# Optimization experiments

Measured on AMD Instinct MI355X. Metric: run time of the kernel, lower is better.

The kernel has to match this reference:

```python
import jax, jax.numpy as jnp
import numpy as np

BETA = 0.95
THRESH = 1.0
T = 25
MAXD = 11      # dilated_kernel_size: 250//25=10 -> bumped to odd 11
LP = 10        # left_pad = 250//25
B = 1024
SIGINIT = 5.0  # max_delay // 2, SIG is frozen at this value


@jax.custom_vjp
def atan_spike(u):
    # heaviside forward, atan surrogate gradient (snntorch surrogate.atan, alpha=2)
    return (u > 0).astype(u.dtype)

def _atan_fwd(u):
    return atan_spike(u), u

def _atan_bwd(u, g):
    return (g / (1.0 + (jnp.pi * u) ** 2),)

atan_spike.defvjp(_atan_fwd, _atan_bwd)


def dcls_kernel(W, P, SIG):
    # DCLS 'gauss': gaussian-interpolated dense kernel.
    # W: (O, I, kc), P/SIG: (1, O, I, kc) -> dense kernel (O, I, MAXD)
    idx = jnp.arange(MAXD, dtype=W.dtype)
    Pc = P[0] + MAXD // 2                      # center positions in dense kernel
    S = jnp.abs(SIG[0]) + 0.27                 # sigma floor (DCLS epsilon)
    X = jnp.exp(-0.5 * ((idx[:, None, None, None] - Pc) / S) ** 2)  # (K,O,I,kc)
    X = X / (X.sum(axis=0, keepdims=True) + 1e-7)
    return jnp.einsum('oic,joic->oij', W, X)


def dcls_conv(x, W, P, SIG, b):
    # x: (B, C_in, L) -> (B, C_out, L - MAXD + 1), VALID conv like padding=0
    k = dcls_kernel(W, P, SIG)
    y = jax.lax.conv_general_dilated(x, k, (1,), 'VALID',
                                     dimension_numbers=('NCH', 'OIH', 'NCH'))
    return y + b[None, :, None]


def batchnorm(x, gamma, beta, mean, var, eps=1e-5):
    # eval-mode BatchNorm1d over (B, C, L)
    inv = gamma / jnp.sqrt(var + eps)
    return (x - mean[None, :, None]) * inv[None, :, None] + beta[None, :, None]


def lif_scan(x):
    # snntorch Leaky, reset_mechanism='subtract'; x: (B, C, T) input currents
    xT = jnp.moveaxis(x, 2, 0)  # (T, B, C)

    def step(mem, xt):
        reset = jax.lax.stop_gradient(atan_spike(mem - THRESH))  # detached reset
        mem = BETA * mem + xt - reset * THRESH
        spk = atan_spike(mem - THRESH)
        return mem, (spk, mem)

    _, (spk, mem) = jax.lax.scan(step, jnp.zeros_like(xT[0]), xT)
    return spk, mem  # each (T, B, C)


def pad_left(x):
    return jnp.pad(x, ((0, 0), (0, 0), (LP, 0)))


def setup_inputs() -> dict:
    key = jax.random.key(0)
    ks = jax.random.split(key, 16)

    def w_init(k, o, i):
        return jax.random.normal(k, (o, i, 1), jnp.float32) / np.sqrt(i)

    inp = {
        'data': jax.random.normal(ks[0], (B, T, 140), jnp.float32),
        'W1': w_init(ks[1], 256, 140),
        'b1': jax.random.normal(ks[2], (256,), jnp.float32) * 0.01,
        'P1': jax.random.uniform(ks[3], (1, 256, 140, 1), jnp.float32, -SIGINIT, SIGINIT),
        'SIG1': jnp.full((1, 256, 140, 1), SIGINIT, jnp.float32),
        'bn1_gamma': jax.random.uniform(ks[4], (256,), jnp.float32, 0.5, 1.5),
        'bn1_beta': jax.random.normal(ks[5], (256,), jnp.float32) * 0.1,
        'bn1_mean': jax.random.normal(ks[6], (256,), jnp.float32) * 0.1,
        'bn1_var': jax.random.uniform(ks[7], (256,), jnp.float32, 0.5, 1.5),
        'W2': w_init(ks[8], 256, 256),
        'b2': jax.random.normal(ks[9], (256,), jnp.float32) * 0.01,
        'P2': jax.random.uniform(ks[10], (1, 256, 256, 1), jnp.float32, -SIGINIT, SIGINIT),
        'SIG2': jnp.full((1, 256, 256, 1), SIGINIT, jnp.float32),
        'bn2_gamma': jax.random.uniform(ks[11], (256,), jnp.float32, 0.5, 1.5),
        'bn2_beta': jax.random.normal(ks[12], (256,), jnp.float32) * 0.1,
        'bn2_mean': jax.random.normal(ks[13], (256,), jnp.float32) * 0.1,
        'bn2_var': jax.random.uniform(ks[14], (256,), jnp.float32, 0.5, 1.5),
        'W3': w_init(ks[15], 20, 256),
        'b3': jnp.zeros((20,), jnp.float32),
        'P3': jax.random.uniform(jax.random.fold_in(key, 99), (1, 20, 256, 1), jnp.float32, -SIGINIT, SIGINIT),
        'SIG3': jnp.full((1, 20, 256, 1), SIGINIT, jnp.float32),
    }
    return inp


def reference(data, W1, b1, P1, SIG1, bn1_gamma, bn1_beta, bn1_mean, bn1_var,
              W2, b2, P2, SIG2, bn2_gamma, bn2_beta, bn2_mean, bn2_var,
              W3, b3, P3, SIG3):
    # data: (B, T, 140); pad time dim on the left, then to (B, C, L)
    x = jnp.moveaxis(jnp.pad(data, ((0, 0), (LP, 0), (0, 0))), 1, 2)  # (B,140,T+LP)
    x = batchnorm(dcls_conv(x, W1, P1, SIG1, b1), bn1_gamma, bn1_beta, bn1_mean, bn1_var)
    spk1, _ = lif_scan(x)                  # (T, B, 256)
    in1 = jnp.moveaxis(spk1, 0, 2)         # (B, 256, T)  (dropout eval = identity)

    x = batchnorm(dcls_conv(pad_left(in1), W2, P2, SIG2, b2),
                  bn2_gamma, bn2_beta, bn2_mean, bn2_var)
    spk2, _ = lif_scan(x)
    in2 = jnp.moveaxis(spk2, 0, 2)         # (B, 256, T)

    x = dcls_conv(pad_left(in2), W3, P3, SIG3, b3)  # (B, 20, T)
    spk3, mem3 = lif_scan(x)               # (T, B, 20) each
    return spk3, mem3
```

## Files before the change

kernel.cpp:

```cpp
#include <hip/hip_runtime.h>
#include <math.h>

#define BB 1024
#define TT 25
#define LP 10
#define MAXD 11

#define XR2 26
#define XC 264
#define XSZ2 (XR2 * XC)

#define IC1 140
#define ICP1 160
#define XC1 168
#define XSZ1 (XR2 * XC1)
#define SS1 (2 * XSZ1)

typedef __bf16 bf16x8 __attribute__((ext_vector_type(8)));
typedef float  f32x4  __attribute__((ext_vector_type(4)));

#define MFMA16(A, B, C) __builtin_amdgcn_mfma_f32_16x16x32_bf16((A), (B), (C), 0, 0, 0)

__global__ void gen_trip(const float* __restrict__ W,
                         const float* __restrict__ P,
                         const float* __restrict__ SIG,
                         __bf16* __restrict__ Khi, __bf16* __restrict__ Kmid,
                         __bf16* __restrict__ Klo,
                         int O, int Opad, int I, int Ipad) {
    int idx = blockIdx.x * blockDim.x + threadIdx.x;
    if (idx >= Opad * Ipad) return;
    int i = idx % Ipad;
    int o = idx / Ipad;
    if (o >= O || i >= I) {
#pragma unroll
        for (int j = 0; j < MAXD; ++j) {
            size_t ofs = ((size_t)(j * Opad + o)) * Ipad + i;
            Khi[ofs] = (__bf16)0.0f;
            Kmid[ofs] = (__bf16)0.0f;
            Klo[ofs] = (__bf16)0.0f;
        }
        return;
    }
    int widx = o * I + i;
    float w  = W[widx];
    float pc = P[widx] + (float)(MAXD / 2);
    float s  = fabsf(SIG[widx]) + 0.27f;
    float x[MAXD];
    float sum = 0.f;
#pragma unroll
    for (int j = 0; j < MAXD; ++j) {
        float d = ((float)j - pc) / s;
        x[j] = expf(-0.5f * d * d);
        sum += x[j];
    }
    float denom = sum + 1e-7f;
#pragma unroll
    for (int j = 0; j < MAXD; ++j) {
        float kv = w * (x[j] / denom);
        __bf16 h = (__bf16)kv;
        float  r1 = kv - (float)h;
        __bf16 m = (__bf16)r1;
        float  r2 = r1 - (float)m;
        __bf16 l = (__bf16)r2;
        size_t ofs = ((size_t)(j * Opad + o)) * Ipad + i;
        Khi[ofs] = h;
        Kmid[ofs] = m;
        Klo[ofs] = l;
    }
}

__global__ __launch_bounds__(512, 2)
void conv1_mfma(const float* __restrict__ xin,
                const __bf16* __restrict__ Khi,
                const __bf16* __restrict__ Kmid,
                const __bf16* __restrict__ Klo,
                const float* __restrict__ bias,
                const float* __restrict__ gamma,
                const float* __restrict__ beta,
                const float* __restrict__ mean,
                const float* __restrict__ var,
                __bf16* __restrict__ spk1) {
    __shared__ __align__(16) char smem[3 * SS1 * 2];
    __bf16* xs = (__bf16*)smem;
    float*  ys = (float*)smem;

    const int rr = blockIdx.x & 7;
    const int gg = blockIdx.x >> 3;
    const int pp = 2 * (rr + 8 * (gg >> 1)) + (gg & 1);
    const int b0 = pp * 2;

    const int tid  = threadIdx.x;
    const int w    = tid >> 6;
    const int lane = tid & 63;
    const int lm   = lane & 15;
    const int quad = lane >> 4;

    {
        uint32_t* xz = (uint32_t*)smem;
        for (int k = tid; k < 3 * SS1 / 2; k += 512) xz[k] = 0u;
    }
    __syncthreads();
#pragma unroll
    for (int bl = 0; bl < 2; ++bl) {
        const float* src = xin + (size_t)(b0 + bl) * (TT * IC1);
        for (int k = tid; k < TT * IC1; k += 512) {
            int t = k / IC1;
            int i = k - t * IC1;
            float x  = src[k];
            __bf16 h = (__bf16)x;
            float r1 = x - (float)h;
            __bf16 m = (__bf16)r1;
            float r2 = r1 - (float)m;
            __bf16 l = (__bf16)r2;
            int ofs = bl * XSZ1 + t * XC1 + i;
            xs[0 * SS1 + ofs] = h;
            xs[1 * SS1 + ofs] = m;
            xs[2 * SS1 + ofs] = l;
        }
    }
    __syncthreads();

    f32x4 acc[2][4];
#pragma unroll
    for (int p = 0; p < 2; ++p)
#pragma unroll
        for (int nt = 0; nt < 4; ++nt) acc[p][nt] = (f32x4){0.f, 0.f, 0.f, 0.f};

    auto loadA = [&](int n, bf16x8* Ah, bf16x8* Am, bf16x8* Al) {
        n = (n > 54) ? 54 : n;
        const int j = n / 5;
        const int ic = n - 5 * j;
        const size_t base =
            (size_t)(j * 256 + w * 32 + lm) * ICP1 + ic * 32 + quad * 8;
#pragma unroll
        for (int p = 0; p < 2; ++p) {
            Ah[p] = *(const bf16x8*)(Khi  + base + p * 16 * ICP1);
            Am[p] = *(const bf16x8*)(Kmid + base + p * 16 * ICP1);
            Al[p] = *(const bf16x8*)(Klo  + base + p * 16 * ICP1);
        }
    };

    auto step = [&](int n, bf16x8* Ah, bf16x8* Am, bf16x8* Al) {
        const int j = n / 5;
        const int ic = n - 5 * j;
        int r0 = lm + j - 10;          r0 = ((unsigned)r0 < 25u) ? r0 : 25;
        int r1 = 16 + lm + j - 10;     r1 = ((unsigned)r1 < 25u) ? r1 : 25;
        const int col = ic * 32 + quad * 8;
#pragma unroll
        for (int bl = 0; bl < 2; ++bl) {
            bf16x8 Bh[2], Bm[2], Bl[2];
#pragma unroll
            for (int th = 0; th < 2; ++th) {
                const int row = th ? r1 : r0;
                const int ofs = bl * XSZ1 + row * XC1 + col;
                Bh[th] = *(const bf16x8*)&xs[0 * SS1 + ofs];
                Bm[th] = *(const bf16x8*)&xs[1 * SS1 + ofs];
                Bl[th] = *(const bf16x8*)&xs[2 * SS1 + ofs];
            }
#pragma unroll
            for (int p = 0; p < 2; ++p)
#pragma unroll
                for (int th = 0; th < 2; ++th)
                    acc[p][bl * 2 + th] = MFMA16(Ah[p], Bh[th], acc[p][bl * 2 + th]);
#pragma unroll
            for (int p = 0; p < 2; ++p)
#pragma unroll
                for (int th = 0; th < 2; ++th)
                    acc[p][bl * 2 + th] = MFMA16(Ah[p], Bm[th], acc[p][bl * 2 + th]);
#pragma unroll
            for (int p = 0; p < 2; ++p)
#pragma unroll
                for (int th = 0; th < 2; ++th)
                    acc[p][bl * 2 + th] = MFMA16(Am[p], Bh[th], acc[p][bl * 2 + th]);
#pragma unroll
            for (int p = 0; p < 2; ++p)
#pragma unroll
                for (int th = 0; th < 2; ++th)
                    acc[p][bl * 2 + th] = MFMA16(Ah[p], Bl[th], acc[p][bl * 2 + th]);
#pragma unroll
            for (int p = 0; p < 2; ++p)
#pragma unroll
                for (int th = 0; th < 2; ++th)
                    acc[p][bl * 2 + th] = MFMA16(Am[p], Bm[th], acc[p][bl * 2 + th]);
#pragma unroll
            for (int p = 0; p < 2; ++p)
#pragma unroll
                for (int th = 0; th < 2; ++th)
                    acc[p][bl * 2 + th] = MFMA16(Al[p], Bh[th], acc[p][bl * 2 + th]);
        }
    };

    bf16x8 A0h[2], A0m[2], A0l[2], A1h[2], A1m[2], A1l[2];
    loadA(0, A0h, A0m, A0l);
    for (int n = 0; n < 54; n += 2) {
        loadA(n + 1, A1h, A1m, A1l);
        step(n, A0h, A0m, A0l);
        loadA(n + 2, A0h, A0m, A0l);
        step(n + 1, A1h, A1m, A1l);
    }
    step(54, A0h, A0m, A0l);

#pragma unroll
    for (int bl = 0; bl < 2; ++bl) {
        __syncthreads();
#pragma unroll
        for (int p = 0; p < 2; ++p)
#pragma unroll
            for (int th = 0; th < 2; ++th) {
                int t = th * 16 + lm;
                if (t < TT) {
                    int ob = w * 32 + p * 16 + quad * 4;
#pragma unroll
                    for (int v = 0; v < 4; ++v)
                        ys[(ob + v) * 27 + t] = acc[p][bl * 2 + th][v];
                }
            }
        __syncthreads();
        if (tid < 256) {
            const int o = tid;
            float scale = gamma[o] / sqrtf(var[o] + 1e-5f);
            float ofs   = (bias[o] - mean[o]) * scale + beta[o];
            unsigned short* dst =
                (unsigned short*)spk1 + (size_t)(b0 + bl) * (TT * 256) + o;
            const float* yrow = &ys[o * 27];
            float memv = 0.f;
#pragma unroll
            for (int t = 0; t < TT; ++t) {
                float a     = yrow[t] * scale + ofs;
                float reset = (memv > 1.0f) ? 1.0f : 0.f;
                memv        = 0.95f * memv + a - reset;
                dst[t * 256] = (memv > 1.0f) ? 0x3F80 : 0;
            }
        }
    }
}

__global__ __launch_bounds__(512, 2)
void conv23_mfma(const __bf16* __restrict__ spk1,
                 const __bf16* __restrict__ Khi,
                 const __bf16* __restrict__ Kmid,
                 const __bf16* __restrict__ Klo,
                 const float* __restrict__ bias,
                 const float* __restrict__ gamma,
                 const float* __restrict__ beta,
                 const float* __restrict__ mean,
                 const float* __restrict__ var,
                 const __bf16* __restrict__ K3hi,
                 const __bf16* __restrict__ K3mid,
                 const __bf16* __restrict__ K3lo,
                 const float* __restrict__ b3,
                 float* __restrict__ out) {
    __shared__ __align__(16) char smem[61568];
    __bf16* xs  = (__bf16*)smem;
    float*  ysq = (float*)(smem + 54912);
    float*  ys3 = (float*)smem;

    const int b0   = blockIdx.x * 4;
    const int tid  = threadIdx.x;
    const int w    = tid >> 6;
    const int lane = tid & 63;
    const int lm   = lane & 15;
    const int quad = lane >> 4;

    for (int k = tid; k < 4 * (XC / 2); k += 512) {
        int bl = k / (XC / 2);
        int c  = k % (XC / 2);
        ((uint32_t*)xs)[(bl * XSZ2 + 25 * XC) / 2 + c] = 0u;
    }
    for (int k = tid; k < 4 * 800; k += 512) {
        int bl = k / 800;
        int v  = k % 800;
        int t  = v >> 5;
        int iv = v & 31;
        uint4 d = ((const uint4*)(spk1 + (size_t)(b0 + bl) * (TT * 256)))[v];
        *(uint4*)&xs[bl * XSZ2 + t * XC + iv * 8] = d;
    }
    __syncthreads();

    f32x4 acc[2][8];
#pragma unroll
    for (int pi = 0; pi < 2; ++pi)
#pragma unroll
        for (int nt = 0; nt < 8; ++nt) acc[pi][nt] = (f32x4){0.f, 0.f, 0.f, 0.f};

    {
        auto loadA = [&](int n, bf16x8* Ah, bf16x8* Am, bf16x8* Al) {
            n = (n > 87) ? 87 : n;
            const int j = n >> 3, ic = n & 7;
#pragma unroll
            for (int pi = 0; pi < 2; ++pi) {
                const size_t base =
                    (size_t)(j * 256 + w * 32 + pi * 16 + lm) * 256 + ic * 32 + quad * 8;
                Ah[pi] = *(const bf16x8*)(Khi  + base);
                Am[pi] = *(const bf16x8*)(Kmid + base);
                Al[pi] = *(const bf16x8*)(Klo  + base);
            }
        };
        auto loadB = [&](int n, bf16x8* Bf) {
            const int j = n >> 3, ic = n & 7;
            int r0 = lm + j - 10;          r0 = ((unsigned)r0 < 25u) ? r0 : 25;
            int r1 = 16 + lm + j - 10;     r1 = ((unsigned)r1 < 25u) ? r1 : 25;
            const int col = ic * 32 + quad * 8;
#pragma unroll
            for (int bl = 0; bl < 4; ++bl) {
                Bf[bl * 2 + 0] = *(const bf16x8*)&xs[bl * XSZ2 + r0 * XC + col];
                Bf[bl * 2 + 1] = *(const bf16x8*)&xs[bl * XSZ2 + r1 * XC + col];
            }
        };
        auto compute = [&](bf16x8* Ah, bf16x8* Am, bf16x8* Al, bf16x8* Bf) {
#pragma unroll
            for (int pi = 0; pi < 2; ++pi)
#pragma unroll
                for (int nt = 0; nt < 8; ++nt)
                    acc[pi][nt] = MFMA16(Ah[pi], Bf[nt], acc[pi][nt]);
#pragma unroll
            for (int pi = 0; pi < 2; ++pi)
#pragma unroll
                for (int nt = 0; nt < 8; ++nt)
                    acc[pi][nt] = MFMA16(Am[pi], Bf[nt], acc[pi][nt]);
#pragma unroll
            for (int pi = 0; pi < 2; ++pi)
#pragma unroll
                for (int nt = 0; nt < 8; ++nt)
                    acc[pi][nt] = MFMA16(Al[pi], Bf[nt], acc[pi][nt]);
        };

        bf16x8 A0h[2], A0m[2], A0l[2], A1h[2], A1m[2], A1l[2], B0[8], B1[8];
        loadA(0, A0h, A0m, A0l);
        loadB(0, B0);
        for (int n = 0; n < 86; n += 2) {
            loadA(n + 1, A1h, A1m, A1l);
            loadB(n + 1, B1);
            compute(A0h, A0m, A0l, B0);
            loadA(n + 2, A0h, A0m, A0l);
            loadB(n + 2, B0);
            compute(A1h, A1m, A1l, B1);
        }
        loadA(87, A1h, A1m, A1l);
        loadB(87, B1);
        compute(A0h, A0m, A0l, B0);
        compute(A1h, A1m, A1l, B1);
    }

#pragma unroll
    for (int bl = 0; bl < 4; ++bl) {
#pragma unroll
        for (int q = 0; q < 4; ++q) {
            __syncthreads();
            if ((w >> 1) == q) {
#pragma unroll
                for (int pi = 0; pi < 2; ++pi)
#pragma unroll
                    for (int th = 0; th < 2; ++th) {
                        int t = th * 16 + lm;
                        if (t < TT) {
                            int ol = (w & 1) * 32 + pi * 16 + quad * 4;
#pragma unroll
                            for (int v = 0; v < 4; ++v)
                                ysq[(ol + v) * 26 + t] = acc[pi][bl * 2 + th][v];
                        }
                    }
            }
            __syncthreads();
            if (tid < 64) {
                const int o = q * 64 + tid;
                float scale = gamma[o] / sqrtf(var[o] + 1e-5f);
                float ofs   = (bias[o] - mean[o]) * scale + beta[o];
                const float* yrow = &ysq[tid * 26];
                unsigned short* sx = (unsigned short*)xs;
                float memv = 0.f;
#pragma unroll
                for (int t = 0; t < TT; ++t) {
                    float a     = yrow[t] * scale + ofs;
                    float reset = (memv > 1.0f) ? 1.0f : 0.f;
                    memv        = 0.95f * memv + a - reset;
                    sx[bl * XSZ2 + t * XC + o] = (memv > 1.0f) ? 0x3F80 : 0;
                }
            }
        }
    }
    __syncthreads();

    {
        const int p3  = w >> 2;
        const int bl3 = w & 3;
        f32x4 accH[2], accM[2], accL[2];
#pragma unroll
        for (int th = 0; th < 2; ++th) {
            accH[th] = (f32x4){0.f, 0.f, 0.f, 0.f};
            accM[th] = (f32x4){0.f, 0.f, 0.f, 0.f};
            accL[th] = (f32x4){0.f, 0.f, 0.f, 0.f};
        }

        auto loadA3 = [&](int n, bf16x8* Ah, bf16x8* Am, bf16x8* Al) {
            n = (n > 87) ? 87 : n;
            const int j = n >> 3, ic = n & 7;
            const size_t kofs =
                ((size_t)(j * 32 + p3 * 16 + lm)) * 256 + ic * 32 + quad * 8;
            *Ah = *(const bf16x8*)(K3hi  + kofs);
            *Am = *(const bf16x8*)(K3mid + kofs);
            *Al = *(const bf16x8*)(K3lo  + kofs);
        };
        auto step3 = [&](int n, bf16x8 Ah, bf16x8 Am, bf16x8 Al) {
            const int j = n >> 3, ic = n & 7;
#pragma unroll
            for (int th = 0; th < 2; ++th) {
                int r = th * 16 + lm + j - 10;
                r = ((unsigned)r < 25u) ? r : 25;
                bf16x8 Bf =
                    *(const bf16x8*)&xs[bl3 * XSZ2 + r * XC + ic * 32 + quad * 8];
                accH[th] = MFMA16(Ah, Bf, accH[th]);
                accM[th] = MFMA16(Am, Bf, accM[th]);
                accL[th] = MFMA16(Al, Bf, accL[th]);
            }
        };

        bf16x8 A0h, A0m, A0l, A1h, A1m, A1l;
        loadA3(0, &A0h, &A0m, &A0l);
        for (int n = 0; n < 86; n += 2) {
            loadA3(n + 1, &A1h, &A1m, &A1l);
            step3(n, A0h, A0m, A0l);
            loadA3(n + 2, &A0h, &A0m, &A0l);
            step3(n + 1, A1h, A1m, A1l);
        }
        loadA3(87, &A1h, &A1m, &A1l);
        step3(86, A0h, A0m, A0l);
        step3(87, A1h, A1m, A1l);

        __syncthreads();
#pragma unroll
        for (int th = 0; th < 2; ++th) {
            int t = th * 16 + lm;
            if (t < TT) {
#pragma unroll
                for (int v = 0; v < 4; ++v)
                    ys3[(bl3 * 32 + p3 * 16 + quad * 4 + v) * 26 + t] =
                        accH[th][v] + accM[th][v] + accL[th][v];
            }
        }
        __syncthreads();

        if (tid < 80) {
            const int bl2 = tid / 20;
            const int o   = tid % 20;
            float memv = 0.f;
            float bo   = b3[o];
            const float* yrow = &ys3[(bl2 * 32 + o) * 26];
#pragma unroll
            for (int t = 0; t < TT; ++t) {
                float a     = yrow[t] + bo;
                float reset = (memv > 1.0f) ? 1.0f : 0.f;
                memv        = 0.95f * memv + a - reset;
                float spk   = (memv > 1.0f) ? 1.0f : 0.f;
                out[(t * BB + (b0 + bl2)) * 20 + o]               = spk;
                out[TT * BB * 20 + (t * BB + (b0 + bl2)) * 20 + o] = memv;
            }
        }
    }
}

extern "C" void kernel_launch(void* const* d_in, const int* in_sizes, int n_in,
                              void* d_out, int out_size, void* d_ws, size_t ws_size,
                              hipStream_t stream) {
    const float* data = (const float*)d_in[0];
    const float* W1   = (const float*)d_in[1];
    const float* b1   = (const float*)d_in[2];
    const float* P1   = (const float*)d_in[3];
    const float* SIG1 = (const float*)d_in[4];
    const float* g1   = (const float*)d_in[5];
    const float* be1  = (const float*)d_in[6];
    const float* m1   = (const float*)d_in[7];
    const float* v1   = (const float*)d_in[8];
    const float* W2   = (const float*)d_in[9];
    const float* b2   = (const float*)d_in[10];
    const float* P2   = (const float*)d_in[11];
    const float* SIG2 = (const float*)d_in[12];
    const float* g2   = (const float*)d_in[13];
    const float* be2  = (const float*)d_in[14];
    const float* m2   = (const float*)d_in[15];
    const float* v2   = (const float*)d_in[16];
    const float* W3   = (const float*)d_in[17];
    const float* b3   = (const float*)d_in[18];
    const float* P3   = (const float*)d_in[19];
    const float* SIG3 = (const float*)d_in[20];
    float* out = (float*)d_out;

    char* p = (char*)d_ws;
    __bf16* K1hi  = (__bf16*)p;  p += 901120;
    __bf16* K1mid = (__bf16*)p;  p += 901120;
    __bf16* K1lo  = (__bf16*)p;  p += 901120;
    __bf16* spk1  = (__bf16*)p;  p += 13107200;
    __bf16* K2hi  = (__bf16*)p;  p += 1441792;
    __bf16* K2mid = (__bf16*)p;  p += 1441792;
    __bf16* K2lo  = (__bf16*)p;  p += 1441792;
    __bf16* K3hi  = (__bf16*)p;  p += 180224;
    __bf16* K3mid = (__bf16*)p;  p += 180224;
    __bf16* K3lo  = (__bf16*)p;

    gen_trip<<<(256 * 160 + 255) / 256, 256, 0, stream>>>(
        W1, P1, SIG1, K1hi, K1mid, K1lo, 256, 256, 140, 160);
    gen_trip<<<(256 * 256 + 255) / 256, 256, 0, stream>>>(
        W2, P2, SIG2, K2hi, K2mid, K2lo, 256, 256, 256, 256);
    gen_trip<<<(32 * 256 + 255) / 256, 256, 0, stream>>>(
        W3, P3, SIG3, K3hi, K3mid, K3lo, 20, 32, 256, 256);

    conv1_mfma<<<BB / 2, 512, 0, stream>>>(data, K1hi, K1mid, K1lo,
                                           b1, g1, be1, m1, v1, spk1);
    conv23_mfma<<<BB / 4, 512, 0, stream>>>(spk1, K2hi, K2mid, K2lo,
                                            b2, g2, be2, m2, v2,
                                            K3hi, K3mid, K3lo, b3, out);
}
```

Baseline: 433.9 us.

## Double conv23 block to 1024 threads, splitting output channels across 16 waves

The fused conv2/conv3 kernel moves from 512 to 1024 threads per block. Each wave now owns 16 output channels instead of 32, which halves its accumulator registers and per-wave A-fragment loads. The conv3 stage is likewise split across time halves per wave. The aim is more waves per block for latency hiding and more MFMA parallelism. In exchange, each wave re-reads the same B fragments from shared memory (more LDS traffic per MFMA), the software double-buffering of B loads is dropped, and launch bounds now allow only one block per CU.

```diff
diff --git a/kernel.cpp b/kernel.cpp
--- a/kernel.cpp
+++ b/kernel.cpp
@@ -235,7 +235,7 @@
     }
 }
 
-__global__ __launch_bounds__(512, 2)
+__global__ __launch_bounds__(1024, 1)
 void conv23_mfma(const __bf16* __restrict__ spk1,
                  const __bf16* __restrict__ Khi,
                  const __bf16* __restrict__ Kmid,
@@ -262,12 +262,12 @@
     const int lm   = lane & 15;
     const int quad = lane >> 4;
 
-    for (int k = tid; k < 4 * (XC / 2); k += 512) {
+    for (int k = tid; k < 4 * (XC / 2); k += 1024) {
         int bl = k / (XC / 2);
         int c  = k % (XC / 2);
         ((uint32_t*)xs)[(bl * XSZ2 + 25 * XC) / 2 + c] = 0u;
     }
-    for (int k = tid; k < 4 * 800; k += 512) {
+    for (int k = tid; k < 4 * 800; k += 1024) {
         int bl = k / 800;
         int v  = k % 800;
         int t  = v >> 5;
@@ -277,69 +277,50 @@
     }
     __syncthreads();
 
-    f32x4 acc[2][8];
-#pragma unroll
-    for (int pi = 0; pi < 2; ++pi)
-#pragma unroll
-        for (int nt = 0; nt < 8; ++nt) acc[pi][nt] = (f32x4){0.f, 0.f, 0.f, 0.f};
+    f32x4 acc[8];
+#pragma unroll
+    for (int nt = 0; nt < 8; ++nt) acc[nt] = (f32x4){0.f, 0.f, 0.f, 0.f};
 
     {
         auto loadA = [&](int n, bf16x8* Ah, bf16x8* Am, bf16x8* Al) {
             n = (n > 87) ? 87 : n;
             const int j = n >> 3, ic = n & 7;
-#pragma unroll
-            for (int pi = 0; pi < 2; ++pi) {
-                const size_t base =
-                    (size_t)(j * 256 + w * 32 + pi * 16 + lm) * 256 + ic * 32 + quad * 8;
-                Ah[pi] = *(const bf16x8*)(Khi  + base);
-                Am[pi] = *(const bf16x8*)(Kmid + base);
-                Al[pi] = *(const bf16x8*)(Klo  + base);
-            }
+            const size_t base =
+                (size_t)(j * 256 + w * 16 + lm) * 256 + ic * 32 + quad * 8;
+            *Ah = *(const bf16x8*)(Khi  + base);
+            *Am = *(const bf16x8*)(Kmid + base);
+            *Al = *(const bf16x8*)(Klo  + base);
         };
-        auto loadB = [&](int n, bf16x8* Bf) {
+        auto step = [&](int n, bf16x8 Ah, bf16x8 Am, bf16x8 Al) {
             const int j = n >> 3, ic = n & 7;
             int r0 = lm + j - 10;          r0 = ((unsigned)r0 < 25u) ? r0 : 25;
             int r1 = 16 + lm + j - 10;     r1 = ((unsigned)r1 < 25u) ? r1 : 25;
             const int col = ic * 32 + quad * 8;
+            bf16x8 Bf[8];
 #pragma unroll
             for (int bl = 0; bl < 4; ++bl) {
                 Bf[bl * 2 + 0] = *(const bf16x8*)&xs[bl * XSZ2 + r0 * XC + col];
                 Bf[bl * 2 + 1] = *(const bf16x8*)&xs[bl * XSZ2 + r1 * XC + col];
             }
+#pragma unroll
+            for (int nt = 0; nt < 8; ++nt) acc[nt] = MFMA16(Ah, Bf[nt], acc[nt]);
+#pragma unroll
+            for (int nt = 0; nt < 8; ++nt) acc[nt] = MFMA16(Am, Bf[nt], acc[nt]);
+#pragma unroll
+            for (int nt = 0; nt < 8; ++nt) acc[nt] = MFMA16(Al, Bf[nt], acc[nt]);
         };
-        auto compute = [&](bf16x8* Ah, bf16x8* Am, bf16x8* Al, bf16x8* Bf) {
-#pragma unroll
-            for (int pi = 0; pi < 2; ++pi)
-#pragma unroll
-                for (int nt = 0; nt < 8; ++nt)
-                    acc[pi][nt] = MFMA16(Ah[pi], Bf[nt], acc[pi][nt]);
-#pragma unroll
-            for (int pi = 0; pi < 2; ++pi)
-#pragma unroll
-                for (int nt = 0; nt < 8; ++nt)
-                    acc[pi][nt] = MFMA16(Am[pi], Bf[nt], acc[pi][nt]);
-#pragma unroll
-            for (int pi = 0; pi < 2; ++pi)
-#pragma unroll
-                for (int nt = 0; nt < 8; ++nt)
-                    acc[pi][nt] = MFMA16(Al[pi], Bf[nt], acc[pi][nt]);
-        };
-
-        bf16x8 A0h[2], A0m[2], A0l[2], A1h[2], A1m[2], A1l[2], B0[8], B1[8];
-        loadA(0, A0h, A0m, A0l);
-        loadB(0, B0);
+
+        bf16x8 A0h, A0m, A0l, A1h, A1m, A1l;
+        loadA(0, &A0h, &A0m, &A0l);
         for (int n = 0; n < 86; n += 2) {
-            loadA(n + 1, A1h, A1m, A1l);
-            loadB(n + 1, B1);
-            compute(A0h, A0m, A0l, B0);
-            loadA(n + 2, A0h, A0m, A0l);
-            loadB(n + 2, B0);
-            compute(A1h, A1m, A1l, B1);
-        }
-        loadA(87, A1h, A1m, A1l);
-        loadB(87, B1);
-        compute(A0h, A0m, A0l, B0);
-        compute(A1h, A1m, A1l, B1);
+            loadA(n + 1, &A1h, &A1m, &A1l);
+            step(n, A0h, A0m, A0l);
+            loadA(n + 2, &A0h, &A0m, &A0l);
+            step(n + 1, A1h, A1m, A1l);
+        }
+        loadA(87, &A1h, &A1m, &A1l);
+        step(86, A0h, A0m, A0l);
+        step(87, A1h, A1m, A1l);
     }
 
 #pragma unroll
@@ -347,19 +328,17 @@
 #pragma unroll
         for (int q = 0; q < 4; ++q) {
             __syncthreads();
-            if ((w >> 1) == q) {
-#pragma unroll
-                for (int pi = 0; pi < 2; ++pi)
-#pragma unroll
-                    for (int th = 0; th < 2; ++th) {
-                        int t = th * 16 + lm;
-                        if (t < TT) {
-                            int ol = (w & 1) * 32 + pi * 16 + quad * 4;
-#pragma unroll
-                            for (int v = 0; v < 4; ++v)
-                                ysq[(ol + v) * 26 + t] = acc[pi][bl * 2 + th][v];
-                        }
+            if ((w >> 2) == q) {
+#pragma unroll
+                for (int th = 0; th < 2; ++th) {
+                    int t = th * 16 + lm;
+                    if (t < TT) {
+                        int ol = (w & 3) * 16 + quad * 4;
+#pragma unroll
+                        for (int v = 0; v < 4; ++v)
+                            ysq[(ol + v) * 26 + t] = acc[bl * 2 + th][v];
                     }
+                }
             }
             __syncthreads();
             if (tid < 64) {
@@ -382,15 +361,13 @@
     __syncthreads();
 
     {
-        const int p3  = w >> 2;
-        const int bl3 = w & 3;
-        f32x4 accH[2], accM[2], accL[2];
-#pragma unroll
-        for (int th = 0; th < 2; ++th) {
-            accH[th] = (f32x4){0.f, 0.f, 0.f, 0.f};
-            accM[th] = (f32x4){0.f, 0.f, 0.f, 0.f};
-            accL[th] = (f32x4){0.f, 0.f, 0.f, 0.f};
-        }
+        const int p3  = w >> 3;
+        const int bl3 = (w >> 1) & 3;
+        const int th3 = w & 1;
+        f32x4 accH, accM, accL;
+        accH = (f32x4){0.f, 0.f, 0.f, 0.f};
+        accM = (f32x4){0.f, 0.f, 0.f, 0.f};
+        accL = (f32x4){0.f, 0.f, 0.f, 0.f};
 
         auto loadA3 = [&](int n, bf16x8* Ah, bf16x8* Am, bf16x8* Al) {
             n = (n > 87) ? 87 : n;
@@ -403,16 +380,13 @@
         };
         auto step3 = [&](int n, bf16x8 Ah, bf16x8 Am, bf16x8 Al) {
             const int j = n >> 3, ic = n & 7;
-#pragma unroll
-            for (int th = 0; th < 2; ++th) {
-                int r = th * 16 + lm + j - 10;
-                r = ((unsigned)r < 25u) ? r : 25;
-                bf16x8 Bf =
-                    *(const bf16x8*)&xs[bl3 * XSZ2 + r * XC + ic * 32 + quad * 8];
-                accH[th] = MFMA16(Ah, Bf, accH[th]);
-                accM[th] = MFMA16(Am, Bf, accM[th]);
-                accL[th] = MFMA16(Al, Bf, accL[th]);
-            }
+            int r = th3 * 16 + lm + j - 10;
+            r = ((unsigned)r < 25u) ? r : 25;
+            bf16x8 Bf =
+                *(const bf16x8*)&xs[bl3 * XSZ2 + r * XC + ic * 32 + quad * 8];
+            accH = MFMA16(Ah, Bf, accH);
+            accM = MFMA16(Am, Bf, accM);
+            accL = MFMA16(Al, Bf, accL);
         };
 
         bf16x8 A0h, A0m, A0l, A1h, A1m, A1l;
@@ -428,14 +402,13 @@
         step3(87, A1h, A1m, A1l);
 
         __syncthreads();
-#pragma unroll
-        for (int th = 0; th < 2; ++th) {
-            int t = th * 16 + lm;
+        {
+            int t = th3 * 16 + lm;
             if (t < TT) {
 #pragma unroll
                 for (int v = 0; v < 4; ++v)
                     ys3[(bl3 * 32 + p3 * 16 + quad * 4 + v) * 26 + t] =
-                        accH[th][v] + accM[th][v] + accL[th][v];
+                        accH[v] + accM[v] + accL[v];
             }
         }
         __syncthreads();
@@ -506,7 +479,7 @@
 
     conv1_mfma<<<BB / 2, 512, 0, stream>>>(data, K1hi, K1mid, K1lo,
                                            b1, g1, be1, m1, v1, spk1);
-    conv23_mfma<<<BB / 4, 512, 0, stream>>>(spk1, K2hi, K2mid, K2lo,
-                                            b2, g2, be2, m2, v2,
-                                            K3hi, K3mid, K3lo, b3, out);
+    conv23_mfma<<<BB / 4, 1024, 0, stream>>>(spk1, K2hi, K2mid, K2lo,
+                                             b2, g2, be2, m2, v2,
+                                             K3hi, K3mid, K3lo, b3, out);
 }
```

Result: slower. 473.5 us (+9.1%).

## Split fused conv2/conv3 kernel and retile conv2 over channel halves and 8 batches

Applied to the files above, without the earlier changes.

The fused conv23 kernel is split into conv2_mfma and conv3_mfma, with layer-2 spikes written to a new global workspace buffer. conv2 now gives each block half of the output channels for 8 batch rows, so each warp loads only its slice of the weight triplets and reuses them across more batch rows. The B fragments are loaded inside each step instead of being double-buffered. This trades an extra kernel launch, a global round trip for spk2, larger LDS per block (about 116KB, which may cap occupancy at one block per CU) and duplicated input staging across the two channel-half blocks, in exchange for more weight reuse per block.

```diff
diff --git a/kernel.cpp b/kernel.cpp
--- a/kernel.cpp
+++ b/kernel.cpp
@@ -236,23 +236,160 @@
 }
 
 __global__ __launch_bounds__(512, 2)
-void conv23_mfma(const __bf16* __restrict__ spk1,
-                 const __bf16* __restrict__ Khi,
-                 const __bf16* __restrict__ Kmid,
-                 const __bf16* __restrict__ Klo,
-                 const float* __restrict__ bias,
-                 const float* __restrict__ gamma,
-                 const float* __restrict__ beta,
-                 const float* __restrict__ mean,
-                 const float* __restrict__ var,
-                 const __bf16* __restrict__ K3hi,
-                 const __bf16* __restrict__ K3mid,
-                 const __bf16* __restrict__ K3lo,
-                 const float* __restrict__ b3,
-                 float* __restrict__ out) {
-    __shared__ __align__(16) char smem[61568];
+void conv2_mfma(const __bf16* __restrict__ spk1,
+                const __bf16* __restrict__ Khi,
+                const __bf16* __restrict__ Kmid,
+                const __bf16* __restrict__ Klo,
+                const float* __restrict__ bias,
+                const float* __restrict__ gamma,
+                const float* __restrict__ beta,
+                const float* __restrict__ mean,
+                const float* __restrict__ var,
+                __bf16* __restrict__ spk2) {
+    __shared__ __align__(16) char smem[116480];
     __bf16* xs  = (__bf16*)smem;
-    float*  ysq = (float*)(smem + 54912);
+    float*  ysq = (float*)(smem + 109824);
+
+    const int h    = blockIdx.x & 1;
+    const int bg   = blockIdx.x >> 1;
+    const int b0   = bg * 8;
+    const int oc0  = h * 128;
+
+    const int tid  = threadIdx.x;
+    const int w    = tid >> 6;
+    const int wc   = w & 3;
+    const int wb   = w >> 2;
+    const int lane = tid & 63;
+    const int lm   = lane & 15;
+    const int quad = lane >> 4;
+
+    for (int k = tid; k < 8 * (XC / 2); k += 512) {
+        int bl = k / (XC / 2);
+        int c  = k % (XC / 2);
+        ((uint32_t*)xs)[(bl * XSZ2 + 25 * XC) / 2 + c] = 0u;
+    }
+    for (int k = tid; k < 8 * 800; k += 512) {
+        int bl = k / 800;
+        int v  = k % 800;
+        int t  = v >> 5;
+        int iv = v & 31;
+        uint4 d = ((const uint4*)(spk1 + (size_t)(b0 + bl) * (TT * 256)))[v];
+        *(uint4*)&xs[bl * XSZ2 + t * XC + iv * 8] = d;
+    }
+    __syncthreads();
+
+    f32x4 acc[2][8];
+#pragma unroll
+    for (int pi = 0; pi < 2; ++pi)
+#pragma unroll
+        for (int nt = 0; nt < 8; ++nt) acc[pi][nt] = (f32x4){0.f, 0.f, 0.f, 0.f};
+
+    {
+        auto loadA = [&](int n, bf16x8* Ah, bf16x8* Am, bf16x8* Al) {
+            n = (n > 87) ? 87 : n;
+            const int j = n >> 3, ic = n & 7;
+#pragma unroll
+            for (int pi = 0; pi < 2; ++pi) {
+                const size_t base =
+                    (size_t)(j * 256 + oc0 + wc * 32 + pi * 16 + lm) * 256 +
+                    ic * 32 + quad * 8;
+                Ah[pi] = *(const bf16x8*)(Khi  + base);
+                Am[pi] = *(const bf16x8*)(Kmid + base);
+                Al[pi] = *(const bf16x8*)(Klo  + base);
+            }
+        };
+        auto step = [&](int n, bf16x8* Ah, bf16x8* Am, bf16x8* Al) {
+            const int j = n >> 3, ic = n & 7;
+            int r0 = lm + j - 10;          r0 = ((unsigned)r0 < 25u) ? r0 : 25;
+            int r1 = 16 + lm + j - 10;     r1 = ((unsigned)r1 < 25u) ? r1 : 25;
+            const int col = ic * 32 + quad * 8;
+            bf16x8 Bf[8];
+#pragma unroll
+            for (int bl = 0; bl < 4; ++bl) {
+                const int xb = wb * 4 + bl;
+                Bf[bl * 2 + 0] = *(const bf16x8*)&xs[xb * XSZ2 + r0 * XC + col];
+                Bf[bl * 2 + 1] = *(const bf16x8*)&xs[xb * XSZ2 + r1 * XC + col];
+            }
+#pragma unroll
+            for (int pi = 0; pi < 2; ++pi)
+#pragma unroll
+                for (int nt = 0; nt < 8; ++nt)
+                    acc[pi][nt] = MFMA16(Ah[pi], Bf[nt], acc[pi][nt]);
+#pragma unroll
+            for (int pi = 0; pi < 2; ++pi)
+#pragma unroll
+                for (int nt = 0; nt < 8; ++nt)
+                    acc[pi][nt] = MFMA16(Am[pi], Bf[nt], acc[pi][nt]);
+#pragma unroll
+            for (int pi = 0; pi < 2; ++pi)
+#pragma unroll
+                for (int nt = 0; nt < 8; ++nt)
+                    acc[pi][nt] = MFMA16(Al[pi], Bf[nt], acc[pi][nt]);
+        };
+
+        bf16x8 A0h[2], A0m[2], A0l[2], A1h[2], A1m[2], A1l[2];
+        loadA(0, A0h, A0m, A0l);
+        for (int n = 0; n < 86; n += 2) {
+            loadA(n + 1, A1h, A1m, A1l);
+            step(n, A0h, A0m, A0l);
+            loadA(n + 2, A0h, A0m, A0l);
+            step(n + 1, A1h, A1m, A1l);
+        }
+        loadA(87, A1h, A1m, A1l);
+        step(86, A0h, A0m, A0l);
+        step(87, A1h, A1m, A1l);
+    }
+
+#pragma unroll
+    for (int blg = 0; blg < 8; ++blg) {
+#pragma unroll
+        for (int q = 0; q < 2; ++q) {
+            __syncthreads();
+            if (wb == (blg >> 2) && (wc >> 1) == q) {
+#pragma unroll
+                for (int pi = 0; pi < 2; ++pi)
+#pragma unroll
+                    for (int th = 0; th < 2; ++th) {
+                        int t = th * 16 + lm;
+                        if (t < TT) {
+                            int ol = (wc & 1) * 32 + pi * 16 + quad * 4;
+#pragma unroll
+                            for (int v = 0; v < 4; ++v)
+                                ysq[(ol + v) * 26 + t] =
+                                    acc[pi][(blg & 3) * 2 + th][v];
+                        }
+                    }
+            }
+            __syncthreads();
+            if (tid < 64) {
+                const int o = oc0 + q * 64 + tid;
+                float scale = gamma[o] / sqrtf(var[o] + 1e-5f);
+                float ofs   = (bias[o] - mean[o]) * scale + beta[o];
+                const float* yrow = &ysq[tid * 26];
+                unsigned short* dst =
+                    (unsigned short*)spk2 + (size_t)(b0 + blg) * (TT * 256) + o;
+                float memv = 0.f;
+#pragma unroll
+                for (int t = 0; t < TT; ++t) {
+                    float a     = yrow[t] * scale + ofs;
+                    float reset = (memv > 1.0f) ? 1.0f : 0.f;
+                    memv        = 0.95f * memv + a - reset;
+                    dst[t * 256] = (memv > 1.0f) ? 0x3F80 : 0;
+                }
+            }
+        }
+    }
+}
+
+__global__ __launch_bounds__(512, 2)
+void conv3_mfma(const __bf16* __restrict__ spk2,
+                const __bf16* __restrict__ K3hi,
+                const __bf16* __restrict__ K3mid,
+                const __bf16* __restrict__ K3lo,
+                const float* __restrict__ b3,
+                float* __restrict__ out) {
+    __shared__ __align__(16) char smem[54912];
+    __bf16* xs  = (__bf16*)smem;
     float*  ys3 = (float*)smem;
 
     const int b0   = blockIdx.x * 4;
@@ -272,112 +409,8 @@
         int v  = k % 800;
         int t  = v >> 5;
         int iv = v & 31;
-        uint4 d = ((const uint4*)(spk1 + (size_t)(b0 + bl) * (TT * 256)))[v];
+        uint4 d = ((const uint4*)(spk2 + (size_t)(b0 + bl) * (TT * 256)))[v];
         *(uint4*)&xs[bl * XSZ2 + t * XC + iv * 8] = d;
-    }
-    __syncthreads();
-
-    f32x4 acc[2][8];
-#pragma unroll
-    for (int pi = 0; pi < 2; ++pi)
-#pragma unroll
-        for (int nt = 0; nt < 8; ++nt) acc[pi][nt] = (f32x4){0.f, 0.f, 0.f, 0.f};
-
-    {
-        auto loadA = [&](int n, bf16x8* Ah, bf16x8* Am, bf16x8* Al) {
-            n = (n > 87) ? 87 : n;
-            const int j = n >> 3, ic = n & 7;
-#pragma unroll
-            for (int pi = 0; pi < 2; ++pi) {
-                const size_t base =
-                    (size_t)(j * 256 + w * 32 + pi * 16 + lm) * 256 + ic * 32 + quad * 8;
-                Ah[pi] = *(const bf16x8*)(Khi  + base);
-                Am[pi] = *(const bf16x8*)(Kmid + base);
-                Al[pi] = *(const bf16x8*)(Klo  + base);
-            }
-        };
-        auto loadB = [&](int n, bf16x8* Bf) {
-            const int j = n >> 3, ic = n & 7;
-            int r0 = lm + j - 10;          r0 = ((unsigned)r0 < 25u) ? r0 : 25;
-            int r1 = 16 + lm + j - 10;     r1 = ((unsigned)r1 < 25u) ? r1 : 25;
-            const int col = ic * 32 + quad * 8;
-#pragma unroll
-            for (int bl = 0; bl < 4; ++bl) {
-                Bf[bl * 2 + 0] = *(const bf16x8*)&xs[bl * XSZ2 + r0 * XC + col];
-                Bf[bl * 2 + 1] = *(const bf16x8*)&xs[bl * XSZ2 + r1 * XC + col];
-            }
-        };
-        auto compute = [&](bf16x8* Ah, bf16x8* Am, bf16x8* Al, bf16x8* Bf) {
-#pragma unroll
-            for (int pi = 0; pi < 2; ++pi)
-#pragma unroll
-                for (int nt = 0; nt < 8; ++nt)
-                    acc[pi][nt] = MFMA16(Ah[pi], Bf[nt], acc[pi][nt]);
-#pragma unroll
-            for (int pi = 0; pi < 2; ++pi)
-#pragma unroll
-                for (int nt = 0; nt < 8; ++nt)
-                    acc[pi][nt] = MFMA16(Am[pi], Bf[nt], acc[pi][nt]);
-#pragma unroll
-            for (int pi = 0; pi < 2; ++pi)
-#pragma unroll
-                for (int nt = 0; nt < 8; ++nt)
-                    acc[pi][nt] = MFMA16(Al[pi], Bf[nt], acc[pi][nt]);
-        };
-
-        bf16x8 A0h[2], A0m[2], A0l[2], A1h[2], A1m[2], A1l[2], B0[8], B1[8];
-        loadA(0, A0h, A0m, A0l);
-        loadB(0, B0);
-        for (int n = 0; n < 86; n += 2) {
-            loadA(n + 1, A1h, A1m, A1l);
-            loadB(n + 1, B1);
-            compute(A0h, A0m, A0l, B0);
-            loadA(n + 2, A0h, A0m, A0l);
-            loadB(n + 2, B0);
-            compute(A1h, A1m, A1l, B1);
-        }
-        loadA(87, A1h, A1m, A1l);
-        loadB(87, B1);
-        compute(A0h, A0m, A0l, B0);
-        compute(A1h, A1m, A1l, B1);
-    }
-
-#pragma unroll
-    for (int bl = 0; bl < 4; ++bl) {
-#pragma unroll
-        for (int q = 0; q < 4; ++q) {
-            __syncthreads();
-            if ((w >> 1) == q) {
-#pragma unroll
-                for (int pi = 0; pi < 2; ++pi)
-#pragma unroll
-                    for (int th = 0; th < 2; ++th) {
-                        int t = th * 16 + lm;
-                        if (t < TT) {
-                            int ol = (w & 1) * 32 + pi * 16 + quad * 4;
-#pragma unroll
-                            for (int v = 0; v < 4; ++v)
-                                ysq[(ol + v) * 26 + t] = acc[pi][bl * 2 + th][v];
-                        }
-                    }
-            }
-            __syncthreads();
-            if (tid < 64) {
-                const int o = q * 64 + tid;
-                float scale = gamma[o] / sqrtf(var[o] + 1e-5f);
-                float ofs   = (bias[o] - mean[o]) * scale + beta[o];
-                const float* yrow = &ysq[tid * 26];
-                unsigned short* sx = (unsigned short*)xs;
-                float memv = 0.f;
-#pragma unroll
-                for (int t = 0; t < TT; ++t) {
-                    float a     = yrow[t] * scale + ofs;
-                    float reset = (memv > 1.0f) ? 1.0f : 0.f;
-                    memv        = 0.95f * memv + a - reset;
-                    sx[bl * XSZ2 + t * XC + o] = (memv > 1.0f) ? 0x3F80 : 0;
-                }
-            }
-        }
     }
     __syncthreads();
 
@@ -495,7 +528,8 @@
     __bf16* K2lo  = (__bf16*)p;  p += 1441792;
     __bf16* K3hi  = (__bf16*)p;  p += 180224;
     __bf16* K3mid = (__bf16*)p;  p += 180224;
-    __bf16* K3lo  = (__bf16*)p;
+    __bf16* K3lo  = (__bf16*)p;  p += 180224;
+    __bf16* spk2  = (__bf16*)p;
 
     gen_trip<<<(256 * 160 + 255) / 256, 256, 0, stream>>>(
         W1, P1, SIG1, K1hi, K1mid, K1lo, 256, 256, 140, 160);
@@ -506,7 +540,7 @@
 
     conv1_mfma<<<BB / 2, 512, 0, stream>>>(data, K1hi, K1mid, K1lo,
                                            b1, g1, be1, m1, v1, spk1);
-    conv23_mfma<<<BB / 4, 512, 0, stream>>>(spk1, K2hi, K2mid, K2lo,
-                                            b2, g2, be2, m2, v2,
-                                            K3hi, K3mid, K3lo, b3, out);
+    conv2_mfma<<<BB / 4, 512, 0, stream>>>(spk1, K2hi, K2mid, K2lo,
+                                           b2, g2, be2, m2, v2, spk2);
+    conv3_mfma<<<BB / 4, 512, 0, stream>>>(spk2, K3hi, K3mid, K3lo, b3, out);
 }
```

New measurement: 432.1 us. Within noise of the previous version (-0.4%).
